# Kernel optimization log

Measured on AMD Instinct MI355X. Metric: run time of the kernel, lower is better.

The kernel has to match this reference:

```python
import jax, jax.numpy as jnp
import numpy as np

N, N_UP, I, L, K = 32, 16, 128, 4, 16
H_S, H_D = 4 * I, 4          # single / double stream widths (512, 4)
F_LEN = 3 * H_S + 2 * H_D    # 1544


def setup_inputs() -> dict:
    key = jax.random.key(0)
    ks = jax.random.split(key, 11)
    f32 = jnp.float32
    return {
        "electron_positions": jax.random.normal(ks[0], (N, 3), f32),
        "nuclei_positions": jax.random.normal(ks[1], (I, 3), f32),
        # torch.rand-style U[0,1) params, scaled to avoid tanh saturation / det overflow
        "v_matrices": jax.random.uniform(ks[2], (L, N, F_LEN, H_S), f32) * 1e-3,
        "b_vectors": jax.random.uniform(ks[3], (L, N, H_S), f32),
        "w_matrices": jax.random.uniform(ks[4], (L, N, N, H_D, H_D), f32) * 0.1,
        "c_vectors": jax.random.uniform(ks[5], (L, N, N, H_D), f32),
        "final_weights": jax.random.uniform(ks[6], (K, N, H_S), f32) * 1e-3,
        "final_biases": jax.random.uniform(ks[7], (K, N), f32),
        "pi_weights": jax.random.uniform(ks[8], (K, N, I), f32) * 1e-2,
        "sigma_weights": jax.random.uniform(ks[9], (K, N, I), f32),
        "omega_weights": jax.random.uniform(ks[10], (K,), f32),
    }


def _fermi_layer(V, b, W, c, sh, dh):
    # sh: [N, H_S], dh: [N, N, H_D]
    g_up = jnp.mean(sh[:N_UP], axis=0)          # [H_S]
    g_dn = jnp.mean(sh[N_UP:], axis=0)          # [H_S]
    dg_up = jnp.mean(dh[:, :N_UP], axis=1)      # [N, H_D]
    dg_dn = jnp.mean(dh[:, N_UP:], axis=1)      # [N, H_D]
    f = jnp.concatenate(
        [sh,
         jnp.broadcast_to(g_up, (N, H_S)),
         jnp.broadcast_to(g_dn, (N, H_S)),
         dg_up, dg_dn], axis=1)                 # [N, F_LEN]
    so = jnp.tanh(jnp.einsum('nfo,nf->no', V, f) + b)      # per-electron matvec
    if so.shape == sh.shape:
        so = so + sh                            # residual (shapes always match here)
    # torch bmm(W[b,i,j], h[b,j]) -> out[b,i] = sum_j W[b,i,j] h[b,j]
    do = jnp.tanh(jnp.einsum('mnij,mnj->mni', W, dh) + c)
    if do.shape == dh.shape:
        do = do + dh
    return so, do


def _forward(electron_positions, nuclei_positions, v_matrices, b_vectors,
             w_matrices, c_vectors, final_weights, final_biases,
             pi_weights, sigma_weights, omega_weights):
    eN = electron_positions[:, None, :] - nuclei_positions[None, :, :]   # [N, I, 3]
    eN_norm = jnp.linalg.norm(eN, axis=-1)                               # [N, I]
    sh = jnp.concatenate([eN.reshape(N, 3 * I), eN_norm], axis=1)        # [N, 4I]
    ee = electron_positions[:, None, :] - electron_positions[None, :, :] # [N, N, 3]
    ee_norm = jnp.linalg.norm(ee, axis=-1, keepdims=True)                # [N, N, 1]
    dh = jnp.concatenate([ee, ee_norm], axis=-1)                         # [N, N, 4]

    # Source quirk: applies layers 0..L-2, then layer L-2 again; layers[-1] unused.
    for li in list(range(L - 1)) + [L - 2]:
        sh, dh = _fermi_layer(v_matrices[li], b_vectors[li],
                              w_matrices[li], c_vectors[li], sh, dh)

    # phi[k,i,j] = (w_ki . h_j + b_ki) * sum_m pi_kim * exp(-||sigma_kim * eN_jm||)
    fd = jnp.einsum('kid,jd->kij', final_weights, sh) + final_biases[:, :, None]
    # ||sigma * v|| = |sigma| * ||v||
    env_exp = jnp.exp(-jnp.abs(sigma_weights)[:, :, None, :]
                      * eN_norm[None, None, :, :])                        # [K,N,N,I]
    env = jnp.einsum('kim,kijm->kij', pi_weights, env_exp)                # [K,N,N]
    phi = fd * env
    d_up = jnp.linalg.det(phi[:, :N_UP, :N_UP])
    d_dn = jnp.linalg.det(phi[:, N_UP:, N_UP:])
    return jnp.sum(omega_weights * d_up * d_dn)


def reference(electron_positions, nuclei_positions, v_matrices, b_vectors,
              w_matrices, c_vectors, final_weights, final_biases,
              pi_weights, sigma_weights, omega_weights):
    return _forward(electron_positions, nuclei_positions, v_matrices, b_vectors,
                    w_matrices, c_vectors, final_weights, final_biases,
                    pi_weights, sigma_weights, omega_weights)
```

## Files before the change

kernel.cpp:

```cpp
#include <hip/hip_runtime.h>
#include <math.h>

#define N_E   32
#define NUP   16
#define N_I   128
#define H_S   512
#define F_LEN 1544
#define N_K   16

#define WS_SH0   0
#define WS_SH1   16384
#define WS_DH0   32768
#define WS_DH1   36864
#define WS_ENN   40960
#define WS_DETS  45056

__global__ __launch_bounds__(256) void k_init(const float* __restrict__ ep,
                                              const float* __restrict__ nuc,
                                              float* __restrict__ ws) {
    float* sh  = ws + WS_SH0;
    float* dh  = ws + WS_DH0;
    float* eNn = ws + WS_ENN;
    int g = blockIdx.x * 256 + threadIdx.x;
    {
        int j = g >> 7, m = g & 127;
        float dx = ep[j*3+0] - nuc[m*3+0];
        float dy = ep[j*3+1] - nuc[m*3+1];
        float dz = ep[j*3+2] - nuc[m*3+2];
        float nr = sqrtf(dx*dx + dy*dy + dz*dz);
        eNn[j*N_I + m] = nr;
        sh[j*H_S + 3*m + 0] = dx;
        sh[j*H_S + 3*m + 1] = dy;
        sh[j*H_S + 3*m + 2] = dz;
        sh[j*H_S + 384 + m] = nr;
    }
    if (g < N_E * N_E) {
        int a = g >> 5, b = g & 31;
        float dx = ep[a*3+0] - ep[b*3+0];
        float dy = ep[a*3+1] - ep[b*3+1];
        float dz = ep[a*3+2] - ep[b*3+2];
        float nr = sqrtf(dx*dx + dy*dy + dz*dz);
        float* d = dh + (a*N_E + b)*4;
        d[0] = dx; d[1] = dy; d[2] = dz; d[3] = nr;
    }
}

__global__ __launch_bounds__(512) void k_mv(const float* __restrict__ V,
                                            const float* __restrict__ sh_in,
                                            float* __restrict__ sh_out,
                                            const float* __restrict__ dh_in,
                                            float* __restrict__ dh_out,
                                            const float* __restrict__ bv,
                                            const float* __restrict__ Wm,
                                            const float* __restrict__ cv,
                                            int li) {
    __shared__ float fv[F_LEN];
    __shared__ float4 part4[16][32];
    int n = blockIdx.x, cg = blockIdx.y, t = threadIdx.x;

    {
        float up = 0.f, dn = 0.f;
        #pragma unroll
        for (int m = 0; m < 16; ++m)  up += sh_in[m*H_S + t];
        #pragma unroll
        for (int m = 16; m < 32; ++m) dn += sh_in[m*H_S + t];
        fv[t]        = sh_in[n*H_S + t];
        fv[512 + t]  = up * 0.0625f;
        fv[1024 + t] = dn * 0.0625f;
        if (t < 4) {
            float s = 0.f;
            #pragma unroll
            for (int j = 0; j < 16; ++j) s += dh_in[(n*N_E + j)*4 + t];
            fv[1536 + t] = s * 0.0625f;
        } else if (t < 8) {
            int i = t - 4; float s = 0.f;
            #pragma unroll
            for (int j = 16; j < 32; ++j) s += dh_in[(n*N_E + j)*4 + i];
            fv[1540 + i] = s * 0.0625f;
        }
    }
    __syncthreads();

    int rbase = ((t >> 6) << 1) | ((t >> 5) & 1);
    int colg  = t & 31;
    const float* Vb = V + ((size_t)(li*N_E + n)*F_LEN)*H_S + cg*128 + colg*4;
    float ax = 0.f, ay = 0.f, az = 0.f, aw = 0.f;
    #pragma unroll 8
    for (int i = 0; i < 96; ++i) {
        int r = i*16 + rbase;
        float4 v4 = *reinterpret_cast<const float4*>(Vb + (size_t)r * H_S);
        float f = fv[r];
        ax = fmaf(v4.x, f, ax);
        ay = fmaf(v4.y, f, ay);
        az = fmaf(v4.z, f, az);
        aw = fmaf(v4.w, f, aw);
    }
    if (rbase < 8) {
        int r = 1536 + rbase;
        float4 v4 = *reinterpret_cast<const float4*>(Vb + (size_t)r * H_S);
        float f = fv[r];
        ax = fmaf(v4.x, f, ax);
        ay = fmaf(v4.y, f, ay);
        az = fmaf(v4.z, f, az);
        aw = fmaf(v4.w, f, aw);
    }
    part4[rbase][colg] = make_float4(ax, ay, az, aw);
    __syncthreads();

    if (t < 32) {
        float sx = 0.f, sy = 0.f, sz = 0.f, sw2 = 0.f;
        #pragma unroll
        for (int g = 0; g < 16; ++g) {
            float4 p = part4[g][t];
            sx += p.x; sy += p.y; sz += p.z; sw2 += p.w;
        }
        int col = cg*128 + t*4;
        const float* bvp = bv + ((size_t)li*N_E + n)*H_S + col;
        const float* sip = sh_in + n*H_S + col;
        float* sop = sh_out + n*H_S + col;
        sop[0] = tanhf(sx  + bvp[0]) + sip[0];
        sop[1] = tanhf(sy  + bvp[1]) + sip[1];
        sop[2] = tanhf(sz  + bvp[2]) + sip[2];
        sop[3] = tanhf(sw2 + bvp[3]) + sip[3];
    }
    if (cg == 0 && t >= 256 && t < 384) {
        int q = t - 256, j2 = q >> 2, ii = q & 3;
        const float* Wp = Wm + ((((size_t)li*N_E + n)*N_E + j2)*4 + ii)*4;
        const float* dr = dh_in + (n*N_E + j2)*4;
        float a2 = Wp[0]*dr[0] + Wp[1]*dr[1] + Wp[2]*dr[2] + Wp[3]*dr[3];
        dh_out[(n*N_E + j2)*4 + ii] =
            tanhf(a2 + cv[(((size_t)li*N_E + n)*N_E + j2)*4 + ii]) + dr[ii];
    }
}

__global__ __launch_bounds__(256) void k_envdet(const float* __restrict__ fw,
                                                const float* __restrict__ fb,
                                                const float* __restrict__ pw,
                                                const float* __restrict__ sw,
                                                const float* __restrict__ sh,
                                                const float* __restrict__ eNn,
                                                float* __restrict__ dets) {
    int b = blockIdx.x, k = b >> 1, sp = b & 1, base = sp * 16;
    int t = threadIdx.x;
    int i = base + (t >> 4);
    int j = base + (t & 15);

    const float* wv = fw + ((size_t)k*N_E + i)*H_S;
    const float* sv = sh + (size_t)j*H_S;
    float fd = 0.f;
    #pragma unroll 8
    for (int c = 0; c < H_S; c += 4) {
        float4 a  = *reinterpret_cast<const float4*>(wv + c);
        float4 bz = *reinterpret_cast<const float4*>(sv + c);
        fd += a.x*bz.x + a.y*bz.y + a.z*bz.z + a.w*bz.w;
    }
    fd += fb[k*N_E + i];

    const float* pv = pw + ((size_t)k*N_E + i)*N_I;
    const float* sg = sw + ((size_t)k*N_E + i)*N_I;
    const float* rn = eNn + (size_t)j*N_I;
    float env = 0.f;
    #pragma unroll 4
    for (int m = 0; m < N_I; ++m)
        env = fmaf(pv[m], expf(-fabsf(sg[m]) * rn[m]), env);

    __shared__ float phi[16][16];
    phi[t >> 4][t & 15] = fd * env;
    __syncthreads();

    if (t < 64) {
        int lane = t;
        int r = lane & 15;
        float a[16];
        #pragma unroll
        for (int c = 0; c < 16; ++c) a[c] = phi[r][c];
        bool used = (lane >= 16);
        float prod = 1.f;
        int sigma[16];
        #pragma unroll
        for (int p = 0; p < 16; ++p) {
            float v = used ? -1.f : fabsf(a[p]);
            int idx = lane;
            #pragma unroll
            for (int off = 32; off; off >>= 1) {
                float ov = __shfl_xor(v, off);
                int   oi = __shfl_xor(idx, off);
                if (ov > v || (ov == v && oi < idx)) { v = ov; idx = oi; }
            }
            int q = idx;
            float pvt = __shfl(a[p], q);
            prod *= pvt;
            sigma[p] = q;
            float factor = (!used && lane != q && pvt != 0.f) ? (a[p] / pvt) : 0.f;
            #pragma unroll
            for (int c = p; c < 16; ++c) {
                float pr = __shfl(a[c], q);
                a[c] -= factor * pr;
            }
            if (lane == q) used = true;
        }
        if (lane == 0) {
            int inv = 0;
            #pragma unroll
            for (int x = 0; x < 16; ++x)
                #pragma unroll
                for (int y = x + 1; y < 16; ++y) inv += (sigma[x] > sigma[y]) ? 1 : 0;
            dets[b] = prod * ((inv & 1) ? -1.f : 1.f);
        }
    }
}

__global__ void k_out(const float* __restrict__ dets, const float* __restrict__ omega,
                      float* __restrict__ out) {
    if (threadIdx.x == 0) {
        float s = 0.f;
        for (int k = 0; k < N_K; ++k)
            s += omega[k] * dets[2*k + 0] * dets[2*k + 1];
        out[0] = s;
    }
}

extern "C" void kernel_launch(void* const* d_in, const int* in_sizes, int n_in,
                              void* d_out, int out_size, void* d_ws, size_t ws_size,
                              hipStream_t stream) {
    const float* ep  = (const float*)d_in[0];
    const float* nuc = (const float*)d_in[1];
    const float* V   = (const float*)d_in[2];
    const float* bv  = (const float*)d_in[3];
    const float* Wm  = (const float*)d_in[4];
    const float* cv  = (const float*)d_in[5];
    const float* fw  = (const float*)d_in[6];
    const float* fb  = (const float*)d_in[7];
    const float* pw  = (const float*)d_in[8];
    const float* sw  = (const float*)d_in[9];
    const float* om  = (const float*)d_in[10];
    float* out = (float*)d_out;
    float* ws  = (float*)d_ws;

    float* shb[2] = { ws + WS_SH0, ws + WS_SH1 };
    float* dhb[2] = { ws + WS_DH0, ws + WS_DH1 };
    float* eNn    = ws + WS_ENN;
    float* dets   = ws + WS_DETS;

    k_init<<<dim3(16), dim3(256), 0, stream>>>(ep, nuc, ws);

    for (int a = 0; a < 4; ++a) {
        int li = (a < 3) ? a : 2;
        k_mv<<<dim3(N_E, 4), dim3(512), 0, stream>>>(
            V, shb[a & 1], shb[(a + 1) & 1], dhb[a & 1], dhb[(a + 1) & 1],
            bv, Wm, cv, li);
    }
    k_envdet<<<dim3(2 * N_K), dim3(256), 0, stream>>>(
        fw, fb, pw, sw, shb[0], eNn, dets);
    k_out<<<dim3(1), dim3(64), 0, stream>>>(dets, om, out);
}
```

Before: 133.3 us.

## Split matvec over more column groups and use nontemporal loads for single-use layers

```diff
diff --git a/kernel.cpp b/kernel.cpp
--- a/kernel.cpp
+++ b/kernel.cpp
@@ -7,6 +7,8 @@
 #define H_S   512
 #define F_LEN 1544
 #define N_K   16
+
+typedef float f32x4 __attribute__((ext_vector_type(4)));
 
 #define WS_SH0   0
 #define WS_SH1   16384
@@ -45,7 +47,8 @@
     }
 }
 
-__global__ __launch_bounds__(512) void k_mv(const float* __restrict__ V,
+template<bool NT>
+__global__ __launch_bounds__(256) void k_mv(const float* __restrict__ V,
                                             const float* __restrict__ sh_in,
                                             float* __restrict__ sh_out,
                                             const float* __restrict__ dh_in,
@@ -55,76 +58,83 @@
                                             const float* __restrict__ cv,
                                             int li) {
     __shared__ float fv[F_LEN];
-    __shared__ float4 part4[16][32];
+    __shared__ f32x4 part4[32][8];
     int n = blockIdx.x, cg = blockIdx.y, t = threadIdx.x;
 
-    {
+    #pragma unroll
+    for (int base = 0; base < 512; base += 256) {
+        int c = base + t;
         float up = 0.f, dn = 0.f;
         #pragma unroll
-        for (int m = 0; m < 16; ++m)  up += sh_in[m*H_S + t];
-        #pragma unroll
-        for (int m = 16; m < 32; ++m) dn += sh_in[m*H_S + t];
-        fv[t]        = sh_in[n*H_S + t];
-        fv[512 + t]  = up * 0.0625f;
-        fv[1024 + t] = dn * 0.0625f;
-        if (t < 4) {
-            float s = 0.f;
-            #pragma unroll
-            for (int j = 0; j < 16; ++j) s += dh_in[(n*N_E + j)*4 + t];
-            fv[1536 + t] = s * 0.0625f;
-        } else if (t < 8) {
-            int i = t - 4; float s = 0.f;
-            #pragma unroll
-            for (int j = 16; j < 32; ++j) s += dh_in[(n*N_E + j)*4 + i];
-            fv[1540 + i] = s * 0.0625f;
+        for (int m = 0; m < 16; ++m)  up += sh_in[m*H_S + c];
+        #pragma unroll
+        for (int m = 16; m < 32; ++m) dn += sh_in[m*H_S + c];
+        fv[c]        = sh_in[n*H_S + c];
+        fv[512 + c]  = up * 0.0625f;
+        fv[1024 + c] = dn * 0.0625f;
+    }
+    if (t < 4) {
+        float s = 0.f;
+        #pragma unroll
+        for (int j = 0; j < 16; ++j) s += dh_in[(n*N_E + j)*4 + t];
+        fv[1536 + t] = s * 0.0625f;
+    } else if (t < 8) {
+        int i = t - 4; float s = 0.f;
+        #pragma unroll
+        for (int j = 16; j < 32; ++j) s += dh_in[(n*N_E + j)*4 + i];
+        fv[1540 + i] = s * 0.0625f;
+    }
+    __syncthreads();
+
+    int rgrp = t >> 3, lane8 = t & 7;
+    const float* Vb = V + ((size_t)(li*N_E + n)*F_LEN)*H_S + cg*32 + lane8*4;
+    f32x4 acc = {0.f, 0.f, 0.f, 0.f};
+    #pragma unroll 16
+    for (int i = 0; i < 48; ++i) {
+        int r = i*32 + rgrp;
+        f32x4 v4;
+        if (NT) v4 = __builtin_nontemporal_load(
+                         reinterpret_cast<const f32x4*>(Vb + (size_t)r * H_S));
+        else    v4 = *reinterpret_cast<const f32x4*>(Vb + (size_t)r * H_S);
+        float f = fv[r];
+        acc.x = fmaf(v4.x, f, acc.x);
+        acc.y = fmaf(v4.y, f, acc.y);
+        acc.z = fmaf(v4.z, f, acc.z);
+        acc.w = fmaf(v4.w, f, acc.w);
+    }
+    if (rgrp < 8) {
+        int r = 1536 + rgrp;
+        f32x4 v4;
+        if (NT) v4 = __builtin_nontemporal_load(
+                         reinterpret_cast<const f32x4*>(Vb + (size_t)r * H_S));
+        else    v4 = *reinterpret_cast<const f32x4*>(Vb + (size_t)r * H_S);
+        float f = fv[r];
+        acc.x = fmaf(v4.x, f, acc.x);
+        acc.y = fmaf(v4.y, f, acc.y);
+        acc.z = fmaf(v4.z, f, acc.z);
+        acc.w = fmaf(v4.w, f, acc.w);
+    }
+    part4[rgrp][lane8] = acc;
+    __syncthreads();
+
+    if (t < 8) {
+        f32x4 s = {0.f, 0.f, 0.f, 0.f};
+        #pragma unroll
+        for (int g = 0; g < 32; ++g) {
+            f32x4 p = part4[g][t];
+            s.x += p.x; s.y += p.y; s.z += p.z; s.w += p.w;
         }
-    }
-    __syncthreads();
-
-    int rbase = ((t >> 6) << 1) | ((t >> 5) & 1);
-    int colg  = t & 31;
-    const float* Vb = V + ((size_t)(li*N_E + n)*F_LEN)*H_S + cg*128 + colg*4;
-    float ax = 0.f, ay = 0.f, az = 0.f, aw = 0.f;
-    #pragma unroll 8
-    for (int i = 0; i < 96; ++i) {
-        int r = i*16 + rbase;
-        float4 v4 = *reinterpret_cast<const float4*>(Vb + (size_t)r * H_S);
-        float f = fv[r];
-        ax = fmaf(v4.x, f, ax);
-        ay = fmaf(v4.y, f, ay);
-        az = fmaf(v4.z, f, az);
-        aw = fmaf(v4.w, f, aw);
-    }
-    if (rbase < 8) {
-        int r = 1536 + rbase;
-        float4 v4 = *reinterpret_cast<const float4*>(Vb + (size_t)r * H_S);
-        float f = fv[r];
-        ax = fmaf(v4.x, f, ax);
-        ay = fmaf(v4.y, f, ay);
-        az = fmaf(v4.z, f, az);
-        aw = fmaf(v4.w, f, aw);
-    }
-    part4[rbase][colg] = make_float4(ax, ay, az, aw);
-    __syncthreads();
-
-    if (t < 32) {
-        float sx = 0.f, sy = 0.f, sz = 0.f, sw2 = 0.f;
-        #pragma unroll
-        for (int g = 0; g < 16; ++g) {
-            float4 p = part4[g][t];
-            sx += p.x; sy += p.y; sz += p.z; sw2 += p.w;
-        }
-        int col = cg*128 + t*4;
+        int col = cg*32 + t*4;
         const float* bvp = bv + ((size_t)li*N_E + n)*H_S + col;
         const float* sip = sh_in + n*H_S + col;
         float* sop = sh_out + n*H_S + col;
-        sop[0] = tanhf(sx  + bvp[0]) + sip[0];
-        sop[1] = tanhf(sy  + bvp[1]) + sip[1];
-        sop[2] = tanhf(sz  + bvp[2]) + sip[2];
-        sop[3] = tanhf(sw2 + bvp[3]) + sip[3];
-    }
-    if (cg == 0 && t >= 256 && t < 384) {
-        int q = t - 256, j2 = q >> 2, ii = q & 3;
+        sop[0] = tanhf(s.x + bvp[0]) + sip[0];
+        sop[1] = tanhf(s.y + bvp[1]) + sip[1];
+        sop[2] = tanhf(s.z + bvp[2]) + sip[2];
+        sop[3] = tanhf(s.w + bvp[3]) + sip[3];
+    }
+    if (cg == 0 && t >= 128 && t < 256) {
+        int q = t - 128, j2 = q >> 2, ii = q & 3;
         const float* Wp = Wm + ((((size_t)li*N_E + n)*N_E + j2)*4 + ii)*4;
         const float* dr = dh_in + (n*N_E + j2)*4;
         float a2 = Wp[0]*dr[0] + Wp[1]*dr[1] + Wp[2]*dr[2] + Wp[3]*dr[3];
@@ -246,9 +256,14 @@
 
     for (int a = 0; a < 4; ++a) {
         int li = (a < 3) ? a : 2;
-        k_mv<<<dim3(N_E, 4), dim3(512), 0, stream>>>(
-            V, shb[a & 1], shb[(a + 1) & 1], dhb[a & 1], dhb[(a + 1) & 1],
-            bv, Wm, cv, li);
+        if (a < 2)
+            k_mv<true><<<dim3(N_E, 16), dim3(256), 0, stream>>>(
+                V, shb[a & 1], shb[(a + 1) & 1], dhb[a & 1], dhb[(a + 1) & 1],
+                bv, Wm, cv, li);
+        else
+            k_mv<false><<<dim3(N_E, 16), dim3(256), 0, stream>>>(
+                V, shb[a & 1], shb[(a + 1) & 1], dhb[a & 1], dhb[(a + 1) & 1],
+                bv, Wm, cv, li);
     }
     k_envdet<<<dim3(2 * N_K), dim3(256), 0, stream>>>(
         fw, fb, pw, sw, shb[0], eNn, dets);
```

After: 136.3 us. 2.2% more time.

## Fuse init into first layer kernel and final reduction into envdet tail

Applied to the files above, without the earlier changes.

```diff
diff --git a/kernel.cpp b/kernel.cpp
--- a/kernel.cpp
+++ b/kernel.cpp
@@ -8,44 +8,20 @@
 #define F_LEN 1544
 #define N_K   16
 
+typedef float f32x4 __attribute__((ext_vector_type(4)));
+
 #define WS_SH0   0
 #define WS_SH1   16384
 #define WS_DH0   32768
 #define WS_DH1   36864
 #define WS_ENN   40960
 #define WS_DETS  45056
-
-__global__ __launch_bounds__(256) void k_init(const float* __restrict__ ep,
-                                              const float* __restrict__ nuc,
-                                              float* __restrict__ ws) {
-    float* sh  = ws + WS_SH0;
-    float* dh  = ws + WS_DH0;
-    float* eNn = ws + WS_ENN;
-    int g = blockIdx.x * 256 + threadIdx.x;
-    {
-        int j = g >> 7, m = g & 127;
-        float dx = ep[j*3+0] - nuc[m*3+0];
-        float dy = ep[j*3+1] - nuc[m*3+1];
-        float dz = ep[j*3+2] - nuc[m*3+2];
-        float nr = sqrtf(dx*dx + dy*dy + dz*dz);
-        eNn[j*N_I + m] = nr;
-        sh[j*H_S + 3*m + 0] = dx;
-        sh[j*H_S + 3*m + 1] = dy;
-        sh[j*H_S + 3*m + 2] = dz;
-        sh[j*H_S + 384 + m] = nr;
-    }
-    if (g < N_E * N_E) {
-        int a = g >> 5, b = g & 31;
-        float dx = ep[a*3+0] - ep[b*3+0];
-        float dy = ep[a*3+1] - ep[b*3+1];
-        float dz = ep[a*3+2] - ep[b*3+2];
-        float nr = sqrtf(dx*dx + dy*dy + dz*dz);
-        float* d = dh + (a*N_E + b)*4;
-        d[0] = dx; d[1] = dy; d[2] = dz; d[3] = nr;
-    }
-}
-
+#define WS_CNT   45088
+
+template<int PHASE>
 __global__ __launch_bounds__(512) void k_mv(const float* __restrict__ V,
+                                            const float* __restrict__ ep,
+                                            const float* __restrict__ nuc,
                                             const float* __restrict__ sh_in,
                                             float* __restrict__ sh_out,
                                             const float* __restrict__ dh_in,
@@ -53,83 +29,134 @@
                                             const float* __restrict__ bv,
                                             const float* __restrict__ Wm,
                                             const float* __restrict__ cv,
+                                            float* __restrict__ ws,
                                             int li) {
     __shared__ float fv[F_LEN];
-    __shared__ float4 part4[16][32];
-    int n = blockIdx.x, cg = blockIdx.y, t = threadIdx.x;
-
-    {
-        float up = 0.f, dn = 0.f;
-        #pragma unroll
-        for (int m = 0; m < 16; ++m)  up += sh_in[m*H_S + t];
-        #pragma unroll
-        for (int m = 16; m < 32; ++m) dn += sh_in[m*H_S + t];
+    __shared__ f32x4 part4[16][32];
+    __shared__ float eps[N_E * 3];
+    int n = blockIdx.x, cgi = blockIdx.y, t = threadIdx.x;
+
+    if (PHASE == 0) {
+        if (t < 96) eps[t] = ep[t];
+        __syncthreads();
+        float self, up, dn;
+        if (t < 384) {
+            int comp = t % 3;
+            float nv = nuc[t];
+            self = eps[n*3 + comp] - nv;
+            float mu = 0.f, md = 0.f;
+            #pragma unroll
+            for (int m2 = 0; m2 < 16; ++m2)  mu += eps[m2*3 + comp] - nv;
+            #pragma unroll
+            for (int m2 = 16; m2 < 32; ++m2) md += eps[m2*3 + comp] - nv;
+            up = mu * 0.0625f; dn = md * 0.0625f;
+        } else {
+            int m = t - 384;
+            float nx = nuc[m*3], ny = nuc[m*3+1], nz = nuc[m*3+2];
+            float su = 0.f, sd = 0.f, own = 0.f;
+            #pragma unroll
+            for (int m2 = 0; m2 < 32; ++m2) {
+                float dx = eps[m2*3]-nx, dy = eps[m2*3+1]-ny, dz = eps[m2*3+2]-nz;
+                float nr = sqrtf(dx*dx + dy*dy + dz*dz);
+                if (m2 < 16) su += nr; else sd += nr;
+                if (m2 == n) own = nr;
+            }
+            self = own; up = su * 0.0625f; dn = sd * 0.0625f;
+            if (cgi == 0) (ws + WS_ENN)[n*N_I + m] = own;
+        }
+        fv[t] = self; fv[512 + t] = up; fv[1024 + t] = dn;
+        if (t < 8) {
+            int comp = t & 3; int j0 = (t < 4) ? 0 : 16;
+            float s = 0.f;
+            for (int j = j0; j < j0 + 16; ++j) {
+                if (comp < 3) s += eps[n*3 + comp] - eps[j*3 + comp];
+                else {
+                    float dx = eps[n*3]-eps[j*3], dy = eps[n*3+1]-eps[j*3+1],
+                          dz = eps[n*3+2]-eps[j*3+2];
+                    s += sqrtf(dx*dx + dy*dy + dz*dz);
+                }
+            }
+            fv[1536 + t] = s * 0.0625f;
+        }
+    } else {
+        float upv = 0.f, dnv = 0.f;
+        #pragma unroll
+        for (int m = 0; m < 16; ++m)  upv += sh_in[m*H_S + t];
+        #pragma unroll
+        for (int m = 16; m < 32; ++m) dnv += sh_in[m*H_S + t];
         fv[t]        = sh_in[n*H_S + t];
-        fv[512 + t]  = up * 0.0625f;
-        fv[1024 + t] = dn * 0.0625f;
-        if (t < 4) {
+        fv[512 + t]  = upv * 0.0625f;
+        fv[1024 + t] = dnv * 0.0625f;
+        if (t < 8) {
+            int comp = t & 3; int j0 = (t < 4) ? 0 : 16;
             float s = 0.f;
             #pragma unroll
-            for (int j = 0; j < 16; ++j) s += dh_in[(n*N_E + j)*4 + t];
+            for (int j = 0; j < 16; ++j) s += dh_in[(n*N_E + j0 + j)*4 + comp];
             fv[1536 + t] = s * 0.0625f;
-        } else if (t < 8) {
-            int i = t - 4; float s = 0.f;
-            #pragma unroll
-            for (int j = 16; j < 32; ++j) s += dh_in[(n*N_E + j)*4 + i];
-            fv[1540 + i] = s * 0.0625f;
-        }
-    }
+        }
+    }
+    if (PHASE == 2 && n == 0 && cgi == 0 && t == 0)
+        *((int*)(ws + WS_CNT)) = 0;
     __syncthreads();
 
     int rbase = ((t >> 6) << 1) | ((t >> 5) & 1);
     int colg  = t & 31;
-    const float* Vb = V + ((size_t)(li*N_E + n)*F_LEN)*H_S + cg*128 + colg*4;
-    float ax = 0.f, ay = 0.f, az = 0.f, aw = 0.f;
+    const float* Vb = V + ((size_t)(li*N_E + n)*F_LEN)*H_S + cgi*128 + colg*4;
+    f32x4 acc = {0.f, 0.f, 0.f, 0.f};
     #pragma unroll 8
     for (int i = 0; i < 96; ++i) {
         int r = i*16 + rbase;
-        float4 v4 = *reinterpret_cast<const float4*>(Vb + (size_t)r * H_S);
+        f32x4 v4 = *reinterpret_cast<const f32x4*>(Vb + (size_t)r * H_S);
         float f = fv[r];
-        ax = fmaf(v4.x, f, ax);
-        ay = fmaf(v4.y, f, ay);
-        az = fmaf(v4.z, f, az);
-        aw = fmaf(v4.w, f, aw);
+        acc.x = fmaf(v4.x, f, acc.x);
+        acc.y = fmaf(v4.y, f, acc.y);
+        acc.z = fmaf(v4.z, f, acc.z);
+        acc.w = fmaf(v4.w, f, acc.w);
     }
     if (rbase < 8) {
         int r = 1536 + rbase;
-        float4 v4 = *reinterpret_cast<const float4*>(Vb + (size_t)r * H_S);
+        f32x4 v4 = *reinterpret_cast<const f32x4*>(Vb + (size_t)r * H_S);
         float f = fv[r];
-        ax = fmaf(v4.x, f, ax);
-        ay = fmaf(v4.y, f, ay);
-        az = fmaf(v4.z, f, az);
-        aw = fmaf(v4.w, f, aw);
-    }
-    part4[rbase][colg] = make_float4(ax, ay, az, aw);
+        acc.x = fmaf(v4.x, f, acc.x);
+        acc.y = fmaf(v4.y, f, acc.y);
+        acc.z = fmaf(v4.z, f, acc.z);
+        acc.w = fmaf(v4.w, f, acc.w);
+    }
+    part4[rbase][colg] = acc;
     __syncthreads();
 
     if (t < 32) {
-        float sx = 0.f, sy = 0.f, sz = 0.f, sw2 = 0.f;
+        f32x4 s = {0.f, 0.f, 0.f, 0.f};
         #pragma unroll
         for (int g = 0; g < 16; ++g) {
-            float4 p = part4[g][t];
-            sx += p.x; sy += p.y; sz += p.z; sw2 += p.w;
-        }
-        int col = cg*128 + t*4;
+            f32x4 p = part4[g][t];
+            s.x += p.x; s.y += p.y; s.z += p.z; s.w += p.w;
+        }
+        int col = cgi*128 + t*4;
         const float* bvp = bv + ((size_t)li*N_E + n)*H_S + col;
-        const float* sip = sh_in + n*H_S + col;
         float* sop = sh_out + n*H_S + col;
-        sop[0] = tanhf(sx  + bvp[0]) + sip[0];
-        sop[1] = tanhf(sy  + bvp[1]) + sip[1];
-        sop[2] = tanhf(sz  + bvp[2]) + sip[2];
-        sop[3] = tanhf(sw2 + bvp[3]) + sip[3];
-    }
-    if (cg == 0 && t >= 256 && t < 384) {
+        sop[0] = tanhf(s.x + bvp[0]) + fv[col+0];
+        sop[1] = tanhf(s.y + bvp[1]) + fv[col+1];
+        sop[2] = tanhf(s.z + bvp[2]) + fv[col+2];
+        sop[3] = tanhf(s.w + bvp[3]) + fv[col+3];
+    }
+    if (cgi == 0 && t >= 256 && t < 384) {
         int q = t - 256, j2 = q >> 2, ii = q & 3;
         const float* Wp = Wm + ((((size_t)li*N_E + n)*N_E + j2)*4 + ii)*4;
-        const float* dr = dh_in + (n*N_E + j2)*4;
-        float a2 = Wp[0]*dr[0] + Wp[1]*dr[1] + Wp[2]*dr[2] + Wp[3]*dr[3];
+        float dr0, dr1, dr2, dr3;
+        if (PHASE == 0) {
+            dr0 = eps[n*3]   - eps[j2*3];
+            dr1 = eps[n*3+1] - eps[j2*3+1];
+            dr2 = eps[n*3+2] - eps[j2*3+2];
+            dr3 = sqrtf(dr0*dr0 + dr1*dr1 + dr2*dr2);
+        } else {
+            const float* drp = dh_in + (n*N_E + j2)*4;
+            dr0 = drp[0]; dr1 = drp[1]; dr2 = drp[2]; dr3 = drp[3];
+        }
+        float a2 = Wp[0]*dr0 + Wp[1]*dr1 + Wp[2]*dr2 + Wp[3]*dr3;
+        float drsel = (ii == 0) ? dr0 : (ii == 1) ? dr1 : (ii == 2) ? dr2 : dr3;
         dh_out[(n*N_E + j2)*4 + ii] =
-            tanhf(a2 + cv[(((size_t)li*N_E + n)*N_E + j2)*4 + ii]) + dr[ii];
+            tanhf(a2 + cv[(((size_t)li*N_E + n)*N_E + j2)*4 + ii]) + drsel;
     }
 }
 
@@ -137,9 +164,13 @@
                                                 const float* __restrict__ fb,
                                                 const float* __restrict__ pw,
                                                 const float* __restrict__ sw,
-                                                const float* __restrict__ sh,
-                                                const float* __restrict__ eNn,
-                                                float* __restrict__ dets) {
+                                                const float* __restrict__ omega,
+                                                float* __restrict__ ws,
+                                                float* __restrict__ out) {
+    const float* sh  = ws + WS_SH0;
+    const float* eNn = ws + WS_ENN;
+    float* dets = ws + WS_DETS;
+    int* cnt = (int*)(ws + WS_CNT);
     int b = blockIdx.x, k = b >> 1, sp = b & 1, base = sp * 16;
     int t = threadIdx.x;
     int i = base + (t >> 4);
@@ -208,14 +239,20 @@
             dets[b] = prod * ((inv & 1) ? -1.f : 1.f);
         }
     }
-}
-
-__global__ void k_out(const float* __restrict__ dets, const float* __restrict__ omega,
-                      float* __restrict__ out) {
-    if (threadIdx.x == 0) {
+    __syncthreads();
+
+    __shared__ int tailFlag;
+    if (t == 0) {
+        __threadfence();
+        int old = atomicAdd(cnt, 1);
+        tailFlag = (old == 31) ? 1 : 0;
+    }
+    __syncthreads();
+    if (tailFlag && t == 0) {
+        __threadfence();
         float s = 0.f;
-        for (int k = 0; k < N_K; ++k)
-            s += omega[k] * dets[2*k + 0] * dets[2*k + 1];
+        for (int kk = 0; kk < N_K; ++kk)
+            s += omega[kk] * dets[2*kk + 0] * dets[2*kk + 1];
         out[0] = s;
     }
 }
@@ -239,18 +276,15 @@
 
     float* shb[2] = { ws + WS_SH0, ws + WS_SH1 };
     float* dhb[2] = { ws + WS_DH0, ws + WS_DH1 };
-    float* eNn    = ws + WS_ENN;
-    float* dets   = ws + WS_DETS;
-
-    k_init<<<dim3(16), dim3(256), 0, stream>>>(ep, nuc, ws);
-
-    for (int a = 0; a < 4; ++a) {
-        int li = (a < 3) ? a : 2;
-        k_mv<<<dim3(N_E, 4), dim3(512), 0, stream>>>(
-            V, shb[a & 1], shb[(a + 1) & 1], dhb[a & 1], dhb[(a + 1) & 1],
-            bv, Wm, cv, li);
-    }
-    k_envdet<<<dim3(2 * N_K), dim3(256), 0, stream>>>(
-        fw, fb, pw, sw, shb[0], eNn, dets);
-    k_out<<<dim3(1), dim3(64), 0, stream>>>(dets, om, out);
+
+    k_mv<0><<<dim3(N_E, 4), dim3(512), 0, stream>>>(
+        V, ep, nuc, shb[0], shb[1], dhb[0], dhb[1], bv, Wm, cv, ws, 0);
+    k_mv<1><<<dim3(N_E, 4), dim3(512), 0, stream>>>(
+        V, ep, nuc, shb[1], shb[0], dhb[1], dhb[0], bv, Wm, cv, ws, 1);
+    k_mv<1><<<dim3(N_E, 4), dim3(512), 0, stream>>>(
+        V, ep, nuc, shb[0], shb[1], dhb[0], dhb[1], bv, Wm, cv, ws, 2);
+    k_mv<2><<<dim3(N_E, 4), dim3(512), 0, stream>>>(
+        V, ep, nuc, shb[1], shb[0], dhb[1], dhb[0], bv, Wm, cv, ws, 2);
+
+    k_envdet<<<dim3(2 * N_K), dim3(256), 0, stream>>>(fw, fb, pw, sw, om, ws, out);
 }
```

Result: faster. 128.6 us (-3.6%).
